# Performance work log

Hardware: AMD Instinct MI355X
Metric: run time of the kernel (lower is better)

The kernel has to match this reference:

```python
import jax, jax.numpy as jnp
import numpy as np

B, NUM_HIDDENS, H, W = 32, 128, 64, 64
EMB_DIM = 64
NUM_EMB = 512
COMMITMENT_COST = 0.25


def setup_inputs() -> dict:
    key = jax.random.key(0)
    ks = jax.random.split(key, 5)
    return {
        "bottom_encoding": jax.random.normal(ks[0], (B, NUM_HIDDENS, H, W), jnp.float32),
        "pre_w": jax.random.normal(ks[1], (EMB_DIM, NUM_HIDDENS), jnp.float32) / np.sqrt(NUM_HIDDENS).astype(np.float32),
        "pre_b": jnp.zeros((EMB_DIM,), jnp.float32),
        "codebook": jax.random.uniform(ks[2], (NUM_EMB, EMB_DIM), jnp.float32, -1.0 / NUM_EMB, 1.0 / NUM_EMB),
        "post_w": jax.random.normal(ks[3], (NUM_HIDDENS, EMB_DIM), jnp.float32) / np.sqrt(EMB_DIM).astype(np.float32),
        "post_b": jnp.zeros((NUM_HIDDENS,), jnp.float32),
    }


def reference(bottom_encoding, pre_w, pre_b, codebook, post_w, post_b):
    # pre-VQ 1x1 conv: [B, num_hiddens, H, W] -> [B, emb_dim, H, W]
    x = jnp.einsum('bchw,oc->bohw', bottom_encoding, pre_w) + pre_b[None, :, None, None]
    # BCHW -> BHWC, flatten to [N, D]
    z = jnp.transpose(x, (0, 2, 3, 1))
    flat = z.reshape(-1, EMB_DIM)
    # squared euclidean distances to codebook: [N, K]
    dists = (jnp.sum(flat * flat, axis=1, keepdims=True)
             + jnp.sum(codebook * codebook, axis=1)[None, :]
             - 2.0 * flat @ codebook.T)
    idx = jnp.argmin(dists, axis=1)              # [N] int
    quantized = codebook[idx].reshape(z.shape)   # gather, [B, H, W, D]
    # VQ losses
    e_latent_loss = jnp.mean((jax.lax.stop_gradient(quantized) - z) ** 2)
    q_latent_loss = jnp.mean((quantized - jax.lax.stop_gradient(z)) ** 2)
    loss = q_latent_loss + COMMITMENT_COST * e_latent_loss
    # straight-through estimator
    quantized_st = z + jax.lax.stop_gradient(quantized - z)
    # perplexity of codebook usage
    counts = jnp.zeros((NUM_EMB,), jnp.float32).at[idx].add(1.0)
    avg_probs = counts / idx.shape[0]
    perplexity = jnp.exp(-jnp.sum(avg_probs * jnp.log(avg_probs + 1e-10)))
    # post-VQ 1x1 conv: [B, emb_dim, H, W] -> [B, num_hiddens, H, W]
    qc = jnp.transpose(quantized_st, (0, 3, 1, 2))
    global_decode = jnp.einsum('bchw,oc->bohw', qc, post_w) + post_b[None, :, None, None]
    indices = idx.reshape(B, H, W)
    return loss, global_decode, perplexity, indices
```

## Files before the change

kernel.cpp:

```cpp
#include <hip/hip_runtime.h>

#define NPX   131072
#define CHN   128
#define HWN   4096
#define EMB   64
#define NCODE 512

#define WS_HIST 0
#define WS_LOSS 2048
#define WS_CC   4096
#define WS_PWT  8192
#define WS_IDX  40960


__global__ __launch_bounds__(512) void vq_prep(const float* __restrict__ preW,
                                               const float* __restrict__ cb,
                                               float* __restrict__ preWT,
                                               float* __restrict__ cc) {
  int t = threadIdx.x;
  for (int i = t; i < CHN * EMB; i += 512) {
    int c = i >> 6, d = i & 63;
    preWT[i] = preW[d * CHN + c];
  }
  if (t < NCODE) {
    const float* row = cb + t * EMB;
    float r[8];
#pragma unroll
    for (int j = 0; j < 8; ++j) r[j] = __fmul_rn(row[j], row[j]);
#pragma unroll
    for (int b = 1; b < 8; ++b)
#pragma unroll
      for (int j = 0; j < 8; ++j)
        r[j] = __fadd_rn(r[j], __fmul_rn(row[b * 8 + j], row[b * 8 + j]));
    cc[t] = __fadd_rn(__fadd_rn(__fadd_rn(r[0], r[1]), __fadd_rn(r[2], r[3])),
                      __fadd_rn(__fadd_rn(r[4], r[5]), __fadd_rn(r[6], r[7])));
  }
}

__global__ __launch_bounds__(256) void vq_pre(const float* __restrict__ A,
                                              const float* __restrict__ preWT,
                                              const float* __restrict__ preB,
                                              float* __restrict__ zbuf) {
  int bid = blockIdx.x;
  int ph = bid & 511, dh = bid >> 9;
  int d0 = dh << 5;
  int p = ph * 256 + threadIdx.x;
  int b = p >> 12, hw = p & 4095;
  const float* Ab = A + (size_t)b * CHN * HWN + hw;

  float z[32];
#pragma unroll
  for (int d = 0; d < 32; ++d) z[d] = 0.f;
  for (int c = 0; c < CHN; c += 4) {
    float a0 = Ab[(size_t)(c + 0) * HWN];
    float a1 = Ab[(size_t)(c + 1) * HWN];
    float a2 = Ab[(size_t)(c + 2) * HWN];
    float a3 = Ab[(size_t)(c + 3) * HWN];
    const float* w = preWT + c * EMB + d0;
#pragma unroll
    for (int d = 0; d < 32; ++d) z[d] = __fadd_rn(z[d], __fmul_rn(a0, w[d]));
    w += EMB;
#pragma unroll
    for (int d = 0; d < 32; ++d) z[d] = __fadd_rn(z[d], __fmul_rn(a1, w[d]));
    w += EMB;
#pragma unroll
    for (int d = 0; d < 32; ++d) z[d] = __fadd_rn(z[d], __fmul_rn(a2, w[d]));
    w += EMB;
#pragma unroll
    for (int d = 0; d < 32; ++d) z[d] = __fadd_rn(z[d], __fmul_rn(a3, w[d]));
  }
#pragma unroll
  for (int d = 0; d < 32; ++d) z[d] = __fadd_rn(z[d], preB[d0 + d]);

  float4* zp = (float4*)(zbuf + (size_t)p * 64 + d0);
#pragma unroll
  for (int i = 0; i < 8; ++i)
    zp[i] = make_float4(z[4 * i + 0], z[4 * i + 1], z[4 * i + 2], z[4 * i + 3]);
}

__global__ __launch_bounds__(256) void vq_search(const float* __restrict__ zbuf,
                                                 const float* __restrict__ cb,
                                                 const float* __restrict__ cc,
                                                 float* __restrict__ bestb,
                                                 int* __restrict__ bidxb) {
  int bid = blockIdx.x;
  int q = bid & 3, ph = bid >> 2;
  int p = ph * 256 + threadIdx.x;

  float z[64];
  const float4* z4 = (const float4*)(zbuf + (size_t)p * 64);
#pragma unroll
  for (int i = 0; i < 16; ++i) {
    float4 v = z4[i];
    z[4 * i + 0] = v.x; z[4 * i + 1] = v.y; z[4 * i + 2] = v.z; z[4 * i + 3] = v.w;
  }

  float r[8];
#pragma unroll
  for (int j = 0; j < 8; ++j) r[j] = __fmul_rn(z[j], z[j]);
#pragma unroll
  for (int bb = 1; bb < 8; ++bb)
#pragma unroll
    for (int j = 0; j < 8; ++j)
      r[j] = __fadd_rn(r[j], __fmul_rn(z[bb * 8 + j], z[bb * 8 + j]));
  float zz = __fadd_rn(__fadd_rn(__fadd_rn(r[0], r[1]), __fadd_rn(r[2], r[3])),
                       __fadd_rn(__fadd_rn(r[4], r[5]), __fadd_rn(r[6], r[7])));

  int k0 = q << 7;
  float best = 3.4e38f;
  int bidx = k0;
  for (int k = k0; k < k0 + 128; ++k) {
    const float* crow = cb + (k << 6);
    float d0 = 0.f, d1 = 0.f, d2 = 0.f, d3 = 0.f;
#pragma unroll
    for (int dd = 0; dd < 64; dd += 4) {
      d0 = fmaf(crow[dd + 0], z[dd + 0], d0);
      d1 = fmaf(crow[dd + 1], z[dd + 1], d1);
      d2 = fmaf(crow[dd + 2], z[dd + 2], d2);
      d3 = fmaf(crow[dd + 3], z[dd + 3], d3);
    }
    float dot = (d0 + d1) + (d2 + d3);
    float dist = __fadd_rn(__fadd_rn(zz, cc[k]), -2.0f * dot);
    if (dist < best) { best = dist; bidx = k; }
  }
  bestb[(size_t)p * 4 + q] = best;
  bidxb[(size_t)p * 4 + q] = bidx;
}

__global__ __launch_bounds__(256) void vq_combine(const float* __restrict__ zbuf,
                                                  const float* __restrict__ cb,
                                                  const float* __restrict__ bestb,
                                                  const int* __restrict__ bidxb,
                                                  float* __restrict__ outIdx,
                                                  int* __restrict__ wsIdx,
                                                  float* __restrict__ lossAcc,
                                                  unsigned int* __restrict__ hist) {
  int p = blockIdx.x * 256 + threadIdx.x;
  float4 bq = ((const float4*)bestb)[p];
  int4 iq = ((const int4*)bidxb)[p];
  float best = bq.x; int bidx = iq.x;
  if (bq.y < best) { best = bq.y; bidx = iq.y; }
  if (bq.z < best) { best = bq.z; bidx = iq.z; }
  if (bq.w < best) { best = bq.w; bidx = iq.w; }

  const float4* q4 = (const float4*)(cb + (bidx << 6));
  const float4* z4 = (const float4*)(zbuf + (size_t)p * 64);
  float ls = 0.f;
#pragma unroll
  for (int i = 0; i < 16; ++i) {
    float4 qv = q4[i];
    float4 zv = z4[i];
    float e;
    e = __fsub_rn(qv.x, zv.x); ls = fmaf(e, e, ls);
    e = __fsub_rn(qv.y, zv.y); ls = fmaf(e, e, ls);
    e = __fsub_rn(qv.z, zv.z); ls = fmaf(e, e, ls);
    e = __fsub_rn(qv.w, zv.w); ls = fmaf(e, e, ls);
  }
#pragma unroll
  for (int off = 32; off; off >>= 1) ls += __shfl_xor(ls, off, 64);
  if ((threadIdx.x & 63) == 0) atomicAdd(lossAcc, ls);
  atomicAdd(&hist[bidx], 1u);
  wsIdx[p] = bidx;
  outIdx[p] = (float)bidx;
}

__global__ __launch_bounds__(256) void vq_decode(const float* __restrict__ cb,
                                                 const int* __restrict__ wsIdx,
                                                 const float* __restrict__ postW,
                                                 const float* __restrict__ postB,
                                                 float* __restrict__ dec) {
  int bid = blockIdx.x;
  int och = bid & 3, ph = bid >> 2;
  int o0 = och << 5;
  int p = ph * 256 + threadIdx.x;
  int b = p >> 12, hw = p & 4095;
  int k = wsIdx[p];
  float qv[64];
  const float4* q4 = (const float4*)(cb + (k << 6));
#pragma unroll
  for (int i = 0; i < 16; ++i) {
    float4 v = q4[i];
    qv[4 * i + 0] = v.x; qv[4 * i + 1] = v.y; qv[4 * i + 2] = v.z; qv[4 * i + 3] = v.w;
  }
  float* out = dec + (size_t)b * CHN * HWN + hw;
  for (int o = o0; o < o0 + 32; ++o) {
    const float* w = postW + o * EMB;
    float a0 = 0.f, a1 = 0.f, a2 = 0.f, a3 = 0.f;
#pragma unroll
    for (int dd = 0; dd < 64; dd += 4) {
      a0 = fmaf(qv[dd + 0], w[dd + 0], a0);
      a1 = fmaf(qv[dd + 1], w[dd + 1], a1);
      a2 = fmaf(qv[dd + 2], w[dd + 2], a2);
      a3 = fmaf(qv[dd + 3], w[dd + 3], a3);
    }
    out[(size_t)o * HWN] = ((a0 + a1) + (a2 + a3)) + postB[o];
  }
}

__global__ __launch_bounds__(512) void vq_final(const unsigned int* __restrict__ hist,
                                                const float* __restrict__ lossAcc,
                                                float* __restrict__ outLoss,
                                                float* __restrict__ outPerp) {
  __shared__ float sred[8];
  int t = threadIdx.x;
  float c = (float)hist[t];
  float pavg = c * (1.0f / 131072.0f);
  float term = pavg * logf(pavg + 1e-10f);
#pragma unroll
  for (int off = 32; off; off >>= 1) term += __shfl_xor(term, off, 64);
  if ((t & 63) == 0) sred[t >> 6] = term;
  __syncthreads();
  if (t == 0) {
    float s = 0.f;
    for (int i = 0; i < 8; ++i) s += sred[i];
    *outPerp = expf(-s);
    *outLoss = 1.25f * (*lossAcc) * (1.0f / 8388608.0f);
  }
}

extern "C" void kernel_launch(void* const* d_in, const int* in_sizes, int n_in,
                              void* d_out, int out_size, void* d_ws, size_t ws_size,
                              hipStream_t stream) {
  const float* A     = (const float*)d_in[0];
  const float* preW  = (const float*)d_in[1];
  const float* preB  = (const float*)d_in[2];
  const float* cb    = (const float*)d_in[3];
  const float* postW = (const float*)d_in[4];
  const float* postB = (const float*)d_in[5];
  float* out = (float*)d_out;

  char* ws = (char*)d_ws;
  unsigned int* hist = (unsigned int*)(ws + WS_HIST);
  float* lossAcc = (float*)(ws + WS_LOSS);
  float* cc      = (float*)(ws + WS_CC);
  float* preWT   = (float*)(ws + WS_PWT);
  int* wsIdx     = (int*)(ws + WS_IDX);

  float* zbuf  = out + 8;
  float* bestb = out + 8388616;
  int*   bidxb = (int*)(out + 8912904);

  hipMemsetAsync(ws, 0, 2052, stream);
  vq_prep<<<1, 512, 0, stream>>>(preW, cb, preWT, cc);
  vq_pre<<<1024, 256, 0, stream>>>(A, preWT, preB, zbuf);
  vq_search<<<2048, 256, 0, stream>>>(zbuf, cb, cc, bestb, bidxb);
  vq_combine<<<512, 256, 0, stream>>>(zbuf, cb, bestb, bidxb,
                                      out + 16777218, wsIdx, lossAcc, hist);
  vq_decode<<<2048, 256, 0, stream>>>(cb, wsIdx, postW, postB, out + 1);
  vq_final<<<1, 512, 0, stream>>>(hist, lossAcc, out, out + 16777217);
}
```

Baseline: 389.4 us.

## Stage weights and codebook in shared memory with register double-buffered prefetch

The pre-conv, search and decode kernels now copy their weight or codebook slice into LDS once per block. Each inner loop then reads float4 vectors from LDS, prefetching the next row into registers while computing on the current one. Before, every thread issued its own scalar uniform global loads per row. The aim is to hide load latency and cut scalar and global memory traffic, at the cost of more registers, an LDS footprint that may reduce occupancy, and a __syncthreads per block.

```diff
diff --git a/kernel.cpp b/kernel.cpp
--- a/kernel.cpp
+++ b/kernel.cpp
@@ -37,10 +37,43 @@
   }
 }
 
+
+#define PRE_ALOAD(AA, CB) { \
+  AA[0] = Ab[(size_t)(((CB) + 0) & 127) * HWN]; \
+  AA[1] = Ab[(size_t)(((CB) + 1) & 127) * HWN]; \
+  AA[2] = Ab[(size_t)(((CB) + 2) & 127) * HWN]; \
+  AA[3] = Ab[(size_t)(((CB) + 3) & 127) * HWN]; }
+
+#define PRE_HALF(av, WB, ZOFF) { \
+  _Pragma("unroll") \
+  for (int j = 0; j < 4; ++j) { \
+    float4 w = WB[j]; \
+    z[(ZOFF) + 4*j + 0] = __fadd_rn(z[(ZOFF) + 4*j + 0], __fmul_rn(av, w.x)); \
+    z[(ZOFF) + 4*j + 1] = __fadd_rn(z[(ZOFF) + 4*j + 1], __fmul_rn(av, w.y)); \
+    z[(ZOFF) + 4*j + 2] = __fadd_rn(z[(ZOFF) + 4*j + 2], __fmul_rn(av, w.z)); \
+    z[(ZOFF) + 4*j + 3] = __fadd_rn(z[(ZOFF) + 4*j + 3], __fmul_rn(av, w.w)); } }
+
+#define PRE_WLOAD(WB, C, HOFF) { \
+  int cw_ = (C) & 127; \
+  _Pragma("unroll") \
+  for (int j = 0; j < 4; ++j) WB[j] = sw[cw_ * 8 + (HOFF) + j]; }
+
+#define PRE_GROUP(AA, CB) { \
+  PRE_HALF(AA[0], W0, 0)  PRE_WLOAD(W0, (CB) + 2, 0) \
+  PRE_HALF(AA[0], W1, 16) PRE_WLOAD(W1, (CB) + 2, 4) \
+  PRE_HALF(AA[1], W2, 0)  PRE_WLOAD(W2, (CB) + 3, 0) \
+  PRE_HALF(AA[1], W3, 16) PRE_WLOAD(W3, (CB) + 3, 4) \
+  PRE_HALF(AA[2], W0, 0)  PRE_WLOAD(W0, (CB) + 4, 0) \
+  PRE_HALF(AA[2], W1, 16) PRE_WLOAD(W1, (CB) + 4, 4) \
+  PRE_HALF(AA[3], W2, 0)  PRE_WLOAD(W2, (CB) + 5, 0) \
+  PRE_HALF(AA[3], W3, 16) PRE_WLOAD(W3, (CB) + 5, 4) }
+
 __global__ __launch_bounds__(256) void vq_pre(const float* __restrict__ A,
                                               const float* __restrict__ preWT,
                                               const float* __restrict__ preB,
                                               float* __restrict__ zbuf) {
+  __shared__ float4 sw[1024];
+  __shared__ float sb[32];
   int bid = blockIdx.x;
   int ph = bid & 511, dh = bid >> 9;
   int d0 = dh << 5;
@@ -48,44 +81,68 @@
   int b = p >> 12, hw = p & 4095;
   const float* Ab = A + (size_t)b * CHN * HWN + hw;
 
+  for (int i = threadIdx.x; i < 1024; i += 256) {
+    int c = i >> 3, j = i & 7;
+    sw[i] = *((const float4*)(preWT + c * EMB + d0) + j);
+  }
+  if (threadIdx.x < 32) sb[threadIdx.x] = preB[d0 + threadIdx.x];
+  __syncthreads();
+
   float z[32];
 #pragma unroll
   for (int d = 0; d < 32; ++d) z[d] = 0.f;
-  for (int c = 0; c < CHN; c += 4) {
-    float a0 = Ab[(size_t)(c + 0) * HWN];
-    float a1 = Ab[(size_t)(c + 1) * HWN];
-    float a2 = Ab[(size_t)(c + 2) * HWN];
-    float a3 = Ab[(size_t)(c + 3) * HWN];
-    const float* w = preWT + c * EMB + d0;
-#pragma unroll
-    for (int d = 0; d < 32; ++d) z[d] = __fadd_rn(z[d], __fmul_rn(a0, w[d]));
-    w += EMB;
-#pragma unroll
-    for (int d = 0; d < 32; ++d) z[d] = __fadd_rn(z[d], __fmul_rn(a1, w[d]));
-    w += EMB;
-#pragma unroll
-    for (int d = 0; d < 32; ++d) z[d] = __fadd_rn(z[d], __fmul_rn(a2, w[d]));
-    w += EMB;
-#pragma unroll
-    for (int d = 0; d < 32; ++d) z[d] = __fadd_rn(z[d], __fmul_rn(a3, w[d]));
-  }
-#pragma unroll
-  for (int d = 0; d < 32; ++d) z[d] = __fadd_rn(z[d], preB[d0 + d]);
+
+  float aA[4], aB[4];
+  PRE_ALOAD(aA, 0)
+  PRE_ALOAD(aB, 4)
+
+  float4 W0[4], W1[4], W2[4], W3[4];
+#pragma unroll
+  for (int j = 0; j < 4; ++j) { W0[j] = sw[j]; W1[j] = sw[4 + j]; W2[j] = sw[8 + j]; W3[j] = sw[12 + j]; }
+
+#pragma unroll 1
+  for (int g2 = 0; g2 < 16; ++g2) {
+    int c0 = g2 * 8;
+    PRE_GROUP(aA, c0)
+    PRE_ALOAD(aA, c0 + 8)
+    PRE_GROUP(aB, c0 + 4)
+    PRE_ALOAD(aB, c0 + 12)
+  }
+
+#pragma unroll
+  for (int d = 0; d < 32; ++d) z[d] = __fadd_rn(z[d], sb[d]);
 
   float4* zp = (float4*)(zbuf + (size_t)p * 64 + d0);
 #pragma unroll
   for (int i = 0; i < 8; ++i)
     zp[i] = make_float4(z[4 * i + 0], z[4 * i + 1], z[4 * i + 2], z[4 * i + 3]);
 }
+
+
+#define SRCH_Q(WB, ZOFF) { \
+  _Pragma("unroll") \
+  for (int j = 0; j < 4; ++j) { \
+    float4 c4 = WB[j]; \
+    d0 = fmaf(c4.x, z[(ZOFF) + 4*j + 0], d0); \
+    d1 = fmaf(c4.y, z[(ZOFF) + 4*j + 1], d1); \
+    d2 = fmaf(c4.z, z[(ZOFF) + 4*j + 2], d2); \
+    d3 = fmaf(c4.w, z[(ZOFF) + 4*j + 3], d3); } }
+
+#define SRCH_L(WB, OFF) { \
+  _Pragma("unroll") \
+  for (int j = 0; j < 4; ++j) WB[j] = nx[(OFF) + j]; }
 
 __global__ __launch_bounds__(256) void vq_search(const float* __restrict__ zbuf,
                                                  const float* __restrict__ cb,
                                                  const float* __restrict__ cc,
                                                  float* __restrict__ bestb,
                                                  int* __restrict__ bidxb) {
+  __shared__ float4 sc[2048];
+  __shared__ float scc[128];
   int bid = blockIdx.x;
   int q = bid & 3, ph = bid >> 2;
   int p = ph * 256 + threadIdx.x;
+  int k0 = q << 7;
 
   float z[64];
   const float4* z4 = (const float4*)(zbuf + (size_t)p * 64);
@@ -94,6 +151,11 @@
     float4 v = z4[i];
     z[4 * i + 0] = v.x; z[4 * i + 1] = v.y; z[4 * i + 2] = v.z; z[4 * i + 3] = v.w;
   }
+
+  const float4* src = (const float4*)(cb + ((size_t)k0 << 6));
+  for (int i = threadIdx.x; i < 2048; i += 256) sc[i] = src[i];
+  if (threadIdx.x < 128) scc[threadIdx.x] = cc[k0 + threadIdx.x];
+  __syncthreads();
 
   float r[8];
 #pragma unroll
@@ -106,22 +168,27 @@
   float zz = __fadd_rn(__fadd_rn(__fadd_rn(r[0], r[1]), __fadd_rn(r[2], r[3])),
                        __fadd_rn(__fadd_rn(r[4], r[5]), __fadd_rn(r[6], r[7])));
 
-  int k0 = q << 7;
+  float4 w0[4], w1[4], w2[4], w3[4];
+#pragma unroll
+  for (int j = 0; j < 4; ++j) { w0[j] = sc[j]; w1[j] = sc[4 + j]; w2[j] = sc[8 + j]; w3[j] = sc[12 + j]; }
+  float ccc = scc[0];
+
   float best = 3.4e38f;
   int bidx = k0;
-  for (int k = k0; k < k0 + 128; ++k) {
-    const float* crow = cb + (k << 6);
+#pragma unroll 1
+  for (int kk = 0; kk < 128; ++kk) {
+    int nk = (kk + 1) & 127;
+    const float4* nx = sc + (nk << 4);
+    float ccn = scc[nk];
     float d0 = 0.f, d1 = 0.f, d2 = 0.f, d3 = 0.f;
-#pragma unroll
-    for (int dd = 0; dd < 64; dd += 4) {
-      d0 = fmaf(crow[dd + 0], z[dd + 0], d0);
-      d1 = fmaf(crow[dd + 1], z[dd + 1], d1);
-      d2 = fmaf(crow[dd + 2], z[dd + 2], d2);
-      d3 = fmaf(crow[dd + 3], z[dd + 3], d3);
-    }
+    SRCH_Q(w0, 0)  SRCH_L(w0, 0)
+    SRCH_Q(w1, 16) SRCH_L(w1, 4)
+    SRCH_Q(w2, 32) SRCH_L(w2, 8)
+    SRCH_Q(w3, 48) SRCH_L(w3, 12)
     float dot = (d0 + d1) + (d2 + d3);
-    float dist = __fadd_rn(__fadd_rn(zz, cc[k]), -2.0f * dot);
-    if (dist < best) { best = dist; bidx = k; }
+    float dist = __fadd_rn(__fadd_rn(zz, ccc), -2.0f * dot);
+    if (dist < best) { best = dist; bidx = k0 + kk; }
+    ccc = ccn;
   }
   bestb[(size_t)p * 4 + q] = best;
   bidxb[(size_t)p * 4 + q] = bidx;
@@ -164,17 +231,34 @@
   outIdx[p] = (float)bidx;
 }
 
+
+#define DEC_Q(WB, ZOFF) { \
+  _Pragma("unroll") \
+  for (int j = 0; j < 4; ++j) { \
+    float4 c4 = WB[j]; \
+    a0 = fmaf(qv[(ZOFF) + 4*j + 0], c4.x, a0); \
+    a1 = fmaf(qv[(ZOFF) + 4*j + 1], c4.y, a1); \
+    a2 = fmaf(qv[(ZOFF) + 4*j + 2], c4.z, a2); \
+    a3 = fmaf(qv[(ZOFF) + 4*j + 3], c4.w, a3); } }
+
+#define DEC_L(WB, OFF) { \
+  _Pragma("unroll") \
+  for (int j = 0; j < 4; ++j) WB[j] = nx[(OFF) + j]; }
+
 __global__ __launch_bounds__(256) void vq_decode(const float* __restrict__ cb,
                                                  const int* __restrict__ wsIdx,
                                                  const float* __restrict__ postW,
                                                  const float* __restrict__ postB,
                                                  float* __restrict__ dec) {
+  __shared__ float4 sw[512];
+  __shared__ float spb[32];
   int bid = blockIdx.x;
   int och = bid & 3, ph = bid >> 2;
   int o0 = och << 5;
   int p = ph * 256 + threadIdx.x;
   int b = p >> 12, hw = p & 4095;
   int k = wsIdx[p];
+
   float qv[64];
   const float4* q4 = (const float4*)(cb + (k << 6));
 #pragma unroll
@@ -182,18 +266,30 @@
     float4 v = q4[i];
     qv[4 * i + 0] = v.x; qv[4 * i + 1] = v.y; qv[4 * i + 2] = v.z; qv[4 * i + 3] = v.w;
   }
+
+  const float4* wsrc = (const float4*)(postW + ((size_t)o0 << 6));
+  for (int i = threadIdx.x; i < 512; i += 256) sw[i] = wsrc[i];
+  if (threadIdx.x < 32) spb[threadIdx.x] = postB[o0 + threadIdx.x];
+  __syncthreads();
+
+  float4 W0[4], W1[4], W2[4], W3[4];
+#pragma unroll
+  for (int j = 0; j < 4; ++j) { W0[j] = sw[j]; W1[j] = sw[4 + j]; W2[j] = sw[8 + j]; W3[j] = sw[12 + j]; }
+  float pbc = spb[0];
+
   float* out = dec + (size_t)b * CHN * HWN + hw;
-  for (int o = o0; o < o0 + 32; ++o) {
-    const float* w = postW + o * EMB;
+#pragma unroll 1
+  for (int oo = 0; oo < 32; ++oo) {
+    int no = (oo + 1) & 31;
+    const float4* nx = sw + (no << 4);
+    float pbn = spb[no];
     float a0 = 0.f, a1 = 0.f, a2 = 0.f, a3 = 0.f;
-#pragma unroll
-    for (int dd = 0; dd < 64; dd += 4) {
-      a0 = fmaf(qv[dd + 0], w[dd + 0], a0);
-      a1 = fmaf(qv[dd + 1], w[dd + 1], a1);
-      a2 = fmaf(qv[dd + 2], w[dd + 2], a2);
-      a3 = fmaf(qv[dd + 3], w[dd + 3], a3);
-    }
-    out[(size_t)o * HWN] = ((a0 + a1) + (a2 + a3)) + postB[o];
+    DEC_Q(W0, 0)  DEC_L(W0, 0)
+    DEC_Q(W1, 16) DEC_L(W1, 4)
+    DEC_Q(W2, 32) DEC_L(W2, 8)
+    DEC_Q(W3, 48) DEC_L(W3, 12)
+    out[(size_t)(o0 + oo) * HWN] = ((a0 + a1) + (a2 + a3)) + pbc;
+    pbc = pbn;
   }
 }
 
```

After: 598.8 us. 53.8% more time.
